# Performance work log

Measured on AMD Instinct MI355X. Metric: run time of the kernel, lower is better.

The kernel has to match this reference:

```python
import jax, jax.numpy as jnp
import numpy as np

B, S, E, D = 8, 2048, 1024, 128  # batch, seq (== max_span), embed_size, att_block_size


def setup_inputs() -> dict:
    key = jax.random.key(0)
    kx, kq, kk, kv = jax.random.split(key, 4)
    x = jax.random.normal(kx, (B, S, E), dtype=jnp.float32)
    # torch nn.Linear weight layout: [out_features, in_features]
    scale = 1.0 / np.sqrt(E)
    Wq = jax.random.normal(kq, (D, E), dtype=jnp.float32) * scale
    Wk = jax.random.normal(kk, (D, E), dtype=jnp.float32) * scale
    Wv = jax.random.normal(kv, (D, E), dtype=jnp.float32) * scale
    return {"x": x, "Wq": Wq, "Wk": Wk, "Wv": Wv}


def reference(x, Wq, Wk, Wv):
    # q/k/v projections: nn.Linear without bias -> x @ W.T
    q = jnp.einsum('bse,de->bsd', x, Wq)  # [B,S,D]
    k = jnp.einsum('bse,de->bsd', x, Wk)
    v = jnp.einsum('bse,de->bsd', x, Wv)

    scores = jnp.einsum('bqd,bkd->bqk', q, k)  # [B,S,S]
    # causal mask (tril): -inf above diagonal
    causal = jnp.tril(jnp.ones((S, S), dtype=bool))
    scores = jnp.where(causal, scores, -jnp.inf)
    # faithful to source: scores divided by sqrt(D) TWICE => effective 1/D
    scores = scores / jnp.float32(D)
    attn = jax.nn.softmax(scores, axis=-1)
    z = jnp.einsum('bqk,bkd->bqd', attn, v)  # [B,S,D]
    return z
```

## Files before the change

### kernel.cpp

```cpp
#include <hip/hip_runtime.h>
#include <cstdint>
#include <cstddef>

#define DEV __device__ __forceinline__

typedef float  f32x4  __attribute__((ext_vector_type(4)));
typedef __bf16 bf16x4 __attribute__((ext_vector_type(4)));
typedef __bf16 bf16x8 __attribute__((ext_vector_type(8)));

constexpr int B = 8, S = 2048, E = 1024, D = 128;
constexpr int M = B * S;

constexpr size_t WS_QKV    = (size_t)3 * M * D;
constexpr size_t WS_F32OFF = WS_QKV + (size_t)3 * D * E;
constexpr size_t WS_NEED   = WS_F32OFF * 2;
constexpr size_t WS_NEED2  = WS_F32OFF * 2 + ((size_t)M * D + M) * 4;
constexpr int    NZ4       = (M * D + M) / 4;

DEV int sniff_is_bf16(const uint32_t* w) {
  int lane = threadIdx.x & 63;
  uint32_t v = w[lane * 1001];
  int e = (v >> 7) & 0xff;
  unsigned long long b = __ballot(e >= 100 && e <= 140);
  return __popcll(b) >= 48;
}

DEV bf16x4 cvt4(float4 f) {
  bf16x4 r; r[0] = (__bf16)f.x; r[1] = (__bf16)f.y; r[2] = (__bf16)f.z; r[3] = (__bf16)f.w;
  return r;
}

DEV void glds16(const void* g, void* l) {
  __builtin_amdgcn_global_load_lds(
      (const __attribute__((address_space(1))) void*)g,
      (__attribute__((address_space(3))) void*)l, 16, 0, 0);
}

__global__ __launch_bounds__(256) void wcast_kernel(
    const void* __restrict__ xp, const void* __restrict__ wqp,
    const void* __restrict__ wkp, const void* __restrict__ wvp,
    unsigned short* __restrict__ wbf, float* __restrict__ zbuf, const int nz4) {
  const int is_b = sniff_is_bf16((const uint32_t*)xp);
  const int row = blockIdx.x;
  const void* src = row < 128 ? wqp : (row < 256 ? wkp : wvp);
  const int r = row & 127;
  const int t = threadIdx.x;
  if (is_b) {
    const uint2* s = (const uint2*)((const unsigned short*)src + (size_t)r * E) + t;
    *((uint2*)(wbf + (size_t)row * E) + t) = *s;
  } else {
    float4 f = *((const float4*)((const float*)src + (size_t)r * E) + t);
    *((bf16x4*)(wbf + (size_t)row * E) + t) = cvt4(f);
  }
  if (nz4) {
    float4 z = {0.f, 0.f, 0.f, 0.f};
    float4* zp = (float4*)zbuf;
    for (int i = blockIdx.x * 256 + t; i < nz4; i += 384 * 256) zp[i] = z;
  }
}

__global__ __launch_bounds__(512, 4) void proj_kernel(
    const void* __restrict__ xp, const void* __restrict__ wqp,
    const void* __restrict__ wkp, const void* __restrict__ wvp,
    const unsigned short* __restrict__ wbf, const int use_wbf,
    unsigned short* __restrict__ ws) {
  __shared__ __align__(16) unsigned short lds[(32 + 384) * 72];
  unsigned short* xbuf = lds;
  unsigned short* wbuf = lds + 32 * 72;

  const int is_b = sniff_is_bf16((const uint32_t*)xp);
  const int m0 = blockIdx.x * 32;

  const int t = threadIdx.x, lane = t & 63, w = t >> 6;
  const int n15 = lane & 15, quad = lane >> 4;
  const int rg = w >> 2, cg = w & 3;

  f32x4 acc[6] = {};
  const int sr = t >> 3, sc8 = (t & 7) * 8;
  const int wr = t >> 3;

  for (int it = 0; it < 16; ++it) {
    const int k0 = it * 64;
    __syncthreads();
    if (t < 256) {
      if (!is_b) {
        const float4* sx = (const float4*)((const float*)xp + (size_t)(m0 + sr) * E + k0 + sc8);
        *(bf16x4*)&xbuf[sr * 72 + sc8] = cvt4(sx[0]);
        *(bf16x4*)&xbuf[sr * 72 + sc8 + 4] = cvt4(sx[1]);
      } else {
        *(uint4*)&xbuf[sr * 72 + sc8] =
            *(const uint4*)((const unsigned short*)xp + (size_t)(m0 + sr) * E + k0 + sc8);
      }
    }
    if (use_wbf) {
#pragma unroll
      for (int j = 0; j < 6; ++j)
        *(uint4*)&wbuf[(j * 64 + wr) * 72 + sc8] =
            *(const uint4*)(wbf + (size_t)(j * 64 + wr) * E + k0 + sc8);
    } else if (!is_b) {
#pragma unroll
      for (int j = 0; j < 6; ++j) {
        const float* wsrc = (j < 2) ? (const float*)wqp : (j < 4) ? (const float*)wkp : (const float*)wvp;
        const int wrow = (j & 1) * 64 + wr;
        const float4* sw = (const float4*)(wsrc + (size_t)wrow * E + k0 + sc8);
        *(bf16x4*)&wbuf[(j * 64 + wr) * 72 + sc8] = cvt4(sw[0]);
        *(bf16x4*)&wbuf[(j * 64 + wr) * 72 + sc8 + 4] = cvt4(sw[1]);
      }
    } else {
#pragma unroll
      for (int j = 0; j < 6; ++j) {
        const unsigned short* wsrc = (j < 2) ? (const unsigned short*)wqp
                                   : (j < 4) ? (const unsigned short*)wkp
                                             : (const unsigned short*)wvp;
        const int wrow = (j & 1) * 64 + wr;
        *(uint4*)&wbuf[(j * 64 + wr) * 72 + sc8] =
            *(const uint4*)(wsrc + (size_t)wrow * E + k0 + sc8);
      }
    }
    __syncthreads();
#pragma unroll
    for (int ks = 0; ks < 2; ++ks) {
      bf16x8 a = *(const bf16x8*)&xbuf[(rg * 16 + n15) * 72 + ks * 32 + quad * 8];
#pragma unroll
      for (int nf = 0; nf < 6; ++nf) {
        bf16x8 bfr = *(const bf16x8*)&wbuf[(cg * 96 + nf * 16 + n15) * 72 + ks * 32 + quad * 8];
        acc[nf] = __builtin_amdgcn_mfma_f32_16x16x32_bf16(a, bfr, acc[nf], 0, 0, 0);
      }
    }
  }

  unsigned short* qws = ws;
  unsigned short* kws = ws + (size_t)M * D;
  unsigned short* vtw = ws + (size_t)2 * M * D;

  __syncthreads();
  unsigned short* tbuf = lds;
#pragma unroll
  for (int nf = 0; nf < 6; ++nf) {
    const int col = cg * 96 + nf * 16 + n15;
    const int self = col >> 7;
    if (self < 2) {
      unsigned short* dst = self ? kws : qws;
      const int gcol = col & 127;
#pragma unroll
      for (int rr = 0; rr < 4; ++rr) {
        const int grow = m0 + rg * 16 + quad * 4 + rr;
        ((__bf16*)dst)[(size_t)grow * D + gcol] = (__bf16)acc[nf][rr];
      }
    } else {
      const int vcol = col - 256;
#pragma unroll
      for (int rr = 0; rr < 4; ++rr)
        ((__bf16*)tbuf)[(rg * 16 + quad * 4 + rr) * 132 + vcol] = (__bf16)acc[nf][rr];
    }
  }
  __syncthreads();
  {
    const int dcol = t >> 2, mst = (t & 3) * 8;
    unsigned short tmp[8] __attribute__((aligned(16)));
#pragma unroll
    for (int j = 0; j < 8; ++j) tmp[j] = tbuf[(mst + j) * 132 + dcol];
    *(uint4*)&vtw[(size_t)dcol * M + m0 + mst] = *(const uint4*)&tmp[0];
  }
}

__global__ __launch_bounds__(256, 2) void attn_seg_kernel(
    const unsigned short* __restrict__ ws, float* __restrict__ ws2,
    float* __restrict__ lws) {
  __shared__ __align__(16) unsigned short kvbuf[2 * 16384];
  __shared__ __align__(16) unsigned short ldsP[4 * 640];

  const int bx = blockIdx.x;
  const int batch = bx & 7;
  const int seg = (bx >> 3) & 1;
  const int t16 = 63 - (bx >> 4);
  const int q0 = t16 * 32;

  const int nch = (q0 + 95) >> 6;
  const int c0 = seg ? ((nch + 1) >> 1) : 0;
  const int c1 = seg ? nch : ((nch + 1) >> 1);
  if (c0 >= c1) return;

  const int t = threadIdx.x, lane = t & 63, s = t >> 6;
  const int qg = s >> 1, kh = s & 1;
  const int n15 = lane & 15, quad = lane >> 4;

  const unsigned short* qws = ws;
  const unsigned short* kws = ws + (size_t)M * D;
  const unsigned short* vtw = ws + (size_t)2 * M * D;
  unsigned short* ldsPw = ldsP + s * 640;

  bf16x8 qf[4];
  {
    const size_t qbase = (size_t)(batch * S + q0 + qg * 16 + n15) * D;
#pragma unroll
    for (int ks = 0; ks < 4; ++ks)
      qf[ks] = *(const bf16x8*)&qws[qbase + ks * 32 + quad * 8];
  }

  const bf16x8 ones = {(__bf16)1.0f, (__bf16)1.0f, (__bf16)1.0f, (__bf16)1.0f,
                       (__bf16)1.0f, (__bf16)1.0f, (__bf16)1.0f, (__bf16)1.0f};

  f32x4 o[8] = {};
  f32x4 lacc = {};

  const int wrow = q0 + qg * 16 + 15;
  const int ncw = (wrow >= kh * 32) ? (((wrow - kh * 32) >> 6) + 1) : 0;

  const int r4 = lane >> 4, c16 = lane & 15;
  const int r8 = lane >> 3, c8 = lane & 7;
  const size_t kgbase = (size_t)(batch * S) * D;
  const size_t vgbase = (size_t)batch * S;

#define STAGE(j0c, b)                                                            \
  {                                                                              \
    unsigned short* kb_ = kvbuf + (b)*16384;                                     \
    unsigned short* vb_ = kb_ + 8192;                                            \
    _Pragma("unroll") for (int j = 0; j < 4; ++j) {                              \
      const int krow = s * 16 + j * 4 + r4;                                      \
      glds16(kws + kgbase + (size_t)((j0c) + krow) * D + ((c16 ^ (krow & 7)) << 3), \
             kb_ + (s * 16 + j * 4) * 128);                                      \
    }                                                                            \
    _Pragma("unroll") for (int j = 0; j < 4; ++j) {                              \
      const int dr = s * 32 + j * 8 + r8;                                        \
      glds16(vtw + (size_t)dr * M + vgbase + (j0c) + ((c8 ^ (dr & 7)) << 3),     \
             vb_ + (s * 32 + j * 8) * 64);                                       \
    }                                                                            \
  }

  STAGE(c0 * 64, c0 & 1);

  for (int c = c0; c < c1; ++c) {
    if (c + 1 < c1) {
      STAGE((c + 1) * 64, (c + 1) & 1);
      asm volatile("s_waitcnt vmcnt(8)" ::: "memory");
    } else {
      asm volatile("s_waitcnt vmcnt(0)" ::: "memory");
    }
    __builtin_amdgcn_s_barrier();

    if (c < ncw) {
      const unsigned short* kb = kvbuf + (c & 1) * 16384;
      const unsigned short* vb = kb + 8192;
      const int xsw = n15 & 7;

      f32x4 sc[2] = {};
      __builtin_amdgcn_s_setprio(1);
#pragma unroll
      for (int nt = 0; nt < 2; ++nt) {
        const int klrow = kh * 32 + nt * 16 + n15;
#pragma unroll
        for (int ks = 0; ks < 4; ++ks) {
          const bf16x8 ka = *(const bf16x8*)&kb[klrow * 128 + (((ks * 4 + quad) ^ xsw) << 3)];
          sc[nt] = __builtin_amdgcn_mfma_f32_16x16x32_bf16(ka, qf[ks], sc[nt], 0, 0, 0);
        }
      }
      __builtin_amdgcn_s_setprio(0);

      const int j0 = c * 64 + kh * 32;
      const bool maskc = (c == ncw - 1);
#pragma unroll
      for (int nt = 0; nt < 2; ++nt) {
        bf16x4 pv;
#pragma unroll
        for (int rr = 0; rr < 4; ++rr) {
          float v = sc[nt][rr] * (1.0f / 128.0f);
          if (maskc && (j0 + nt * 16 + quad * 4 + rr > q0 + qg * 16 + n15)) v = -1e30f;
          pv[rr] = (__bf16)__expf(v);
        }
        *(bf16x4*)&ldsPw[n15 * 40 + nt * 16 + quad * 4] = pv;
      }

      const bf16x8 pa = *(const bf16x8*)&ldsPw[n15 * 40 + quad * 8];
      __builtin_amdgcn_s_setprio(1);
#pragma unroll
      for (int dn = 0; dn < 8; ++dn) {
        const bf16x8 vfr =
            *(const bf16x8*)&vb[(dn * 16 + n15) * 64 + (((kh * 4 + quad) ^ xsw) << 3)];
        o[dn] = __builtin_amdgcn_mfma_f32_16x16x32_bf16(pa, vfr, o[dn], 0, 0, 0);
      }
      lacc = __builtin_amdgcn_mfma_f32_16x16x32_bf16(pa, ones, lacc, 0, 0, 0);
      __builtin_amdgcn_s_setprio(0);
    }

    __builtin_amdgcn_s_barrier();
  }
#undef STAGE

  float* obase = ws2 + (size_t)(batch * S + q0) * D;
#pragma unroll
  for (int dn = 0; dn < 8; ++dn)
#pragma unroll
    for (int rr = 0; rr < 4; ++rr)
      atomicAdd(&obase[(size_t)(qg * 16 + quad * 4 + rr) * D + dn * 16 + n15], o[dn][rr]);
  if (n15 == 0)
#pragma unroll
    for (int rr = 0; rr < 4; ++rr)
      atomicAdd(&lws[batch * S + q0 + qg * 16 + quad * 4 + rr], lacc[rr]);
}

__global__ __launch_bounds__(256, 2) void attn_kernel(
    const void* __restrict__ xp, const unsigned short* __restrict__ ws,
    void* __restrict__ outp) {
  __shared__ __align__(16) unsigned short kvbuf[2 * 16384];
  __shared__ __align__(16) unsigned short ldsP[4 * 640];
  __shared__ float lbuf[32];
  __shared__ int cnt2[2];

  const int is_b = sniff_is_bf16((const uint32_t*)xp);
  const int bx = blockIdx.x;
  const int batch = bx & 7;
  const int g8 = (bx & 255) >> 3;
  const int t16 = (bx < 256) ? (63 - g8) : g8;
  const int q0 = t16 * 32;
  const int t = threadIdx.x, lane = t & 63, s = t >> 6;
  const int qg = s >> 1, kh = s & 1;
  const int n15 = lane & 15, quad = lane >> 4;

  const unsigned short* qws = ws;
  const unsigned short* kws = ws + (size_t)M * D;
  const unsigned short* vtw = ws + (size_t)2 * M * D;
  unsigned short* ldsPw = ldsP + s * 640;

  if (t < 2) cnt2[t] = 0;

  bf16x8 qf[4];
  {
    const size_t qbase = (size_t)(batch * S + q0 + qg * 16 + n15) * D;
#pragma unroll
    for (int ks = 0; ks < 4; ++ks)
      qf[ks] = *(const bf16x8*)&qws[qbase + ks * 32 + quad * 8];
  }

  const bf16x8 ones = {(__bf16)1.0f, (__bf16)1.0f, (__bf16)1.0f, (__bf16)1.0f,
                       (__bf16)1.0f, (__bf16)1.0f, (__bf16)1.0f, (__bf16)1.0f};

  f32x4 o[8] = {};
  f32x4 lacc = {};

  const int nch = (q0 + 95) >> 6;
  const int wrow = q0 + qg * 16 + 15;
  const int ncw = (wrow >= kh * 32) ? (((wrow - kh * 32) >> 6) + 1) : 0;

  const int r4 = lane >> 4, c16 = lane & 15;
  const int r8 = lane >> 3, c8 = lane & 7;
  const size_t kgbase = (size_t)(batch * S) * D;
  const size_t vgbase = (size_t)batch * S;

#define STAGE(j0c, b)                                                            \
  {                                                                              \
    unsigned short* kb_ = kvbuf + (b)*16384;                                     \
    unsigned short* vb_ = kb_ + 8192;                                            \
    _Pragma("unroll") for (int j = 0; j < 4; ++j) {                              \
      const int krow = s * 16 + j * 4 + r4;                                      \
      glds16(kws + kgbase + (size_t)((j0c) + krow) * D + ((c16 ^ (krow & 7)) << 3), \
             kb_ + (s * 16 + j * 4) * 128);                                      \
    }                                                                            \
    _Pragma("unroll") for (int j = 0; j < 4; ++j) {                              \
      const int dr = s * 32 + j * 8 + r8;                                        \
      glds16(vtw + (size_t)dr * M + vgbase + (j0c) + ((c8 ^ (dr & 7)) << 3),     \
             vb_ + (s * 32 + j * 8) * 64);                                       \
    }                                                                            \
  }

  STAGE(0, 0);

  for (int c = 0; c < nch; ++c) {
    if (c + 1 < nch) {
      STAGE((c + 1) * 64, (c + 1) & 1);
      asm volatile("s_waitcnt vmcnt(8)" ::: "memory");
    } else {
      asm volatile("s_waitcnt vmcnt(0)" ::: "memory");
    }
    __builtin_amdgcn_s_barrier();

    if (c < ncw) {
      const unsigned short* kb = kvbuf + (c & 1) * 16384;
      const unsigned short* vb = kb + 8192;
      const int xsw = n15 & 7;

      f32x4 sc[2] = {};
      __builtin_amdgcn_s_setprio(1);
#pragma unroll
      for (int nt = 0; nt < 2; ++nt) {
        const int klrow = kh * 32 + nt * 16 + n15;
#pragma unroll
        for (int ks = 0; ks < 4; ++ks) {
          const bf16x8 ka = *(const bf16x8*)&kb[klrow * 128 + (((ks * 4 + quad) ^ xsw) << 3)];
          sc[nt] = __builtin_amdgcn_mfma_f32_16x16x32_bf16(ka, qf[ks], sc[nt], 0, 0, 0);
        }
      }
      __builtin_amdgcn_s_setprio(0);

      const int j0 = c * 64 + kh * 32;
      const bool maskc = (c == ncw - 1);
#pragma unroll
      for (int nt = 0; nt < 2; ++nt) {
        bf16x4 pv;
#pragma unroll
        for (int rr = 0; rr < 4; ++rr) {
          float v = sc[nt][rr] * (1.0f / 128.0f);
          if (maskc && (j0 + nt * 16 + quad * 4 + rr > q0 + qg * 16 + n15)) v = -1e30f;
          pv[rr] = (__bf16)__expf(v);
        }
        *(bf16x4*)&ldsPw[n15 * 40 + nt * 16 + quad * 4] = pv;
      }

      const bf16x8 pa = *(const bf16x8*)&ldsPw[n15 * 40 + quad * 8];
      __builtin_amdgcn_s_setprio(1);
#pragma unroll
      for (int dn = 0; dn < 8; ++dn) {
        const bf16x8 vfr =
            *(const bf16x8*)&vb[(dn * 16 + n15) * 64 + (((kh * 4 + quad) ^ xsw) << 3)];
        o[dn] = __builtin_amdgcn_mfma_f32_16x16x32_bf16(pa, vfr, o[dn], 0, 0, 0);
      }
      lacc = __builtin_amdgcn_mfma_f32_16x16x32_bf16(pa, ones, lacc, 0, 0, 0);
      __builtin_amdgcn_s_setprio(0);
    }

    __builtin_amdgcn_s_barrier();
  }
#undef STAGE

  __syncthreads();

  float* Obuf = (float*)kvbuf;
  if (kh == 0) {
#pragma unroll
    for (int dn = 0; dn < 8; ++dn)
#pragma unroll
      for (int rr = 0; rr < 4; ++rr)
        Obuf[(qg * 16 + quad * 4 + rr) * 132 + dn * 16 + n15] = o[dn][rr];
    if (n15 == 0)
#pragma unroll
      for (int rr = 0; rr < 4; ++rr)
        lbuf[qg * 16 + quad * 4 + rr] = lacc[rr];
    asm volatile("" ::: "memory");
    if (lane == 0) atomicAdd(&cnt2[qg], 1);
  } else {
    while (__hip_atomic_load(&cnt2[qg], __ATOMIC_RELAXED, __HIP_MEMORY_SCOPE_WORKGROUP) < 1)
      __builtin_amdgcn_s_sleep(1);
    asm volatile("" ::: "memory");
#pragma unroll
    for (int dn = 0; dn < 8; ++dn)
#pragma unroll
      for (int rr = 0; rr < 4; ++rr)
        atomicAdd(&Obuf[(qg * 16 + quad * 4 + rr) * 132 + dn * 16 + n15], o[dn][rr]);
    if (n15 == 0)
#pragma unroll
      for (int rr = 0; rr < 4; ++rr)
        atomicAdd(&lbuf[qg * 16 + quad * 4 + rr], lacc[rr]);
    if (lane == 0) atomicAdd(&cnt2[qg], 1);
  }
  while (__hip_atomic_load(&cnt2[0], __ATOMIC_RELAXED, __HIP_MEMORY_SCOPE_WORKGROUP) < 2 ||
         __hip_atomic_load(&cnt2[1], __ATOMIC_RELAXED, __HIP_MEMORY_SCOPE_WORKGROUP) < 2)
    __builtin_amdgcn_s_sleep(1);
  asm volatile("" ::: "memory");

  {
    const int row = t >> 3, cb = (t & 7) * 16;
    const float invl = 1.0f / lbuf[row];
    const size_t grow = (size_t)(batch * S + q0 + row) * D;
    if (is_b) {
#pragma unroll
      for (int i = 0; i < 16; ++i)
        ((__bf16*)outp)[grow + cb + i] = (__bf16)(Obuf[row * 132 + cb + i] * invl);
    } else {
#pragma unroll
      for (int i = 0; i < 16; ++i)
        ((float*)outp)[grow + cb + i] = Obuf[row * 132 + cb + i] * invl;
    }
  }
}

__global__ __launch_bounds__(256) void finalize_kernel(
    const void* __restrict__ xp, const float* __restrict__ ws2,
    const float* __restrict__ lws, void* __restrict__ outp) {
  const int is_b = sniff_is_bf16((const uint32_t*)xp);
  const size_t g = ((size_t)blockIdx.x * 256 + threadIdx.x) * 8;
  const int m = (int)(g >> 7);
  const float invl = 1.0f / lws[m];
  float4 a = *(const float4*)(ws2 + g);
  float4 b2 = *(const float4*)(ws2 + g + 4);
  if (is_b) {
    bf16x8 r;
    r[0] = (__bf16)(a.x * invl);  r[1] = (__bf16)(a.y * invl);
    r[2] = (__bf16)(a.z * invl);  r[3] = (__bf16)(a.w * invl);
    r[4] = (__bf16)(b2.x * invl); r[5] = (__bf16)(b2.y * invl);
    r[6] = (__bf16)(b2.z * invl); r[7] = (__bf16)(b2.w * invl);
    *(bf16x8*)((__bf16*)outp + g) = r;
  } else {
    float4 ra = {a.x * invl, a.y * invl, a.z * invl, a.w * invl};
    float4 rb = {b2.x * invl, b2.y * invl, b2.z * invl, b2.w * invl};
    *(float4*)((float*)outp + g) = ra;
    *(float4*)((float*)outp + g + 4) = rb;
  }
}

extern "C" void kernel_launch(void* const* d_in, const int* in_sizes, int n_in,
                              void* d_out, int out_size, void* d_ws, size_t ws_size,
                              hipStream_t stream) {
  (void)in_sizes; (void)n_in; (void)out_size;
  const void* x  = d_in[0];
  const void* wq = d_in[1];
  const void* wk = d_in[2];
  const void* wv = d_in[3];
  unsigned short* ws = (unsigned short*)d_ws;
  unsigned short* wbf = ws + WS_QKV;
  float* ws2 = (float*)(ws + WS_F32OFF);
  float* lws = ws2 + (size_t)M * D;
  const int use_wbf = (ws_size >= WS_NEED) ? 1 : 0;
  const int use_seg = (ws_size >= WS_NEED2) ? 1 : 0;

  if (use_wbf)
    wcast_kernel<<<dim3(384), dim3(256), 0, stream>>>(x, wq, wk, wv, wbf, ws2,
                                                      use_seg ? NZ4 : 0);
  proj_kernel<<<dim3(512), dim3(512), 0, stream>>>(x, wq, wk, wv, wbf, use_wbf, ws);
  if (use_seg) {
    attn_seg_kernel<<<dim3(1024), dim3(256), 0, stream>>>(ws, ws2, lws);
    finalize_kernel<<<dim3(1024), dim3(256), 0, stream>>>(x, ws2, lws, d_out);
  } else {
    attn_kernel<<<dim3(512), dim3(256), 0, stream>>>(x, ws, d_out);
  }
}
```

Before: 174.8 us.

## Double-buffer projection GEMM with direct global-to-LDS loads and XOR swizzle

Rewrites the QKV projection main loop for the bf16-input fast path. It now double-buffers the x and weight tiles in LDS using direct global-to-LDS loads (glds16), with vmcnt waits and raw barriers, so the next tile's loads overlap the current MFMAs. LDS padding is replaced by an XOR swizzle to avoid bank conflicts. The larger shared buffer lowers the occupancy hint from 4 to 2 blocks per CU, which may reduce latency hiding. The fast path only runs when the input is detected as bf16; fp32 inputs take the swizzled single-buffer fallback.

```diff
diff --git a/kernel.cpp b/kernel.cpp
--- a/kernel.cpp
+++ b/kernel.cpp
@@ -59,82 +59,121 @@
   }
 }
 
-__global__ __launch_bounds__(512, 4) void proj_kernel(
+__global__ __launch_bounds__(512, 2) void proj_kernel(
     const void* __restrict__ xp, const void* __restrict__ wqp,
     const void* __restrict__ wkp, const void* __restrict__ wvp,
     const unsigned short* __restrict__ wbf, const int use_wbf,
     unsigned short* __restrict__ ws) {
-  __shared__ __align__(16) unsigned short lds[(32 + 384) * 72];
-  unsigned short* xbuf = lds;
-  unsigned short* wbuf = lds + 32 * 72;
+  __shared__ __align__(16) unsigned short xw[2 * 26624];
 
   const int is_b = sniff_is_bf16((const uint32_t*)xp);
   const int m0 = blockIdx.x * 32;
 
-  const int t = threadIdx.x, lane = t & 63, w = t >> 6;
+  const int t = threadIdx.x, lane = t & 63, s = t >> 6;
   const int n15 = lane & 15, quad = lane >> 4;
-  const int rg = w >> 2, cg = w & 3;
+  const int rg = s >> 2, cg = s & 3;
+  const int xsw = n15 & 7;
 
   f32x4 acc[6] = {};
-  const int sr = t >> 3, sc8 = (t & 7) * 8;
-  const int wr = t >> 3;
-
-  for (int it = 0; it < 16; ++it) {
-    const int k0 = it * 64;
-    __syncthreads();
-    if (t < 256) {
-      if (!is_b) {
-        const float4* sx = (const float4*)((const float*)xp + (size_t)(m0 + sr) * E + k0 + sc8);
-        *(bf16x4*)&xbuf[sr * 72 + sc8] = cvt4(sx[0]);
-        *(bf16x4*)&xbuf[sr * 72 + sc8 + 4] = cvt4(sx[1]);
+
+#define PMFMA(xb_, wb_)                                                         \
+  {                                                                             \
+    _Pragma("unroll") for (int ks = 0; ks < 2; ++ks) {                          \
+      bf16x8 a = *(const bf16x8*)&(xb_)[(rg * 16 + n15) * 64 +                  \
+                                        (((ks * 4 + quad) ^ xsw) << 3)];        \
+      _Pragma("unroll") for (int nf = 0; nf < 6; ++nf) {                        \
+        const int wc = cg * 96 + nf * 16 + n15;                                 \
+        bf16x8 bb = *(const bf16x8*)&(wb_)[wc * 64 +                            \
+                                           (((ks * 4 + quad) ^ xsw) << 3)];     \
+        acc[nf] = __builtin_amdgcn_mfma_f32_16x16x32_bf16(a, bb, acc[nf], 0, 0, 0); \
+      }                                                                         \
+    }                                                                           \
+  }
+
+  if (is_b && use_wbf) {
+#define PSTAGE(k0_, b_)                                                          \
+  {                                                                              \
+    unsigned short* xd = xw + (b_) * 26624 + s * 256;                            \
+    unsigned short* wd = xw + (b_) * 26624 + 2048;                               \
+    if (lane < 32) {                                                             \
+      const int xr = s * 4 + (lane >> 3);                                        \
+      glds16((const unsigned short*)xp + (size_t)(m0 + xr) * E + (k0_) +         \
+                 (((lane & 7) ^ (xr & 7)) << 3),                                 \
+             xd);                                                                \
+    }                                                                            \
+    _Pragma("unroll") for (int j = 0; j < 6; ++j) {                              \
+      const int wr_ = (s * 6 + j) * 8 + (lane >> 3);                             \
+      glds16(wbf + (size_t)wr_ * E + (k0_) + (((lane & 7) ^ (wr_ & 7)) << 3),    \
+             wd + (s * 6 + j) * 512);                                            \
+    }                                                                            \
+  }
+    PSTAGE(0, 0);
+    for (int it = 0; it < 16; ++it) {
+      if (it + 1 < 16) {
+        PSTAGE((it + 1) * 64, (it + 1) & 1);
+        asm volatile("s_waitcnt vmcnt(7)" ::: "memory");
       } else {
-        *(uint4*)&xbuf[sr * 72 + sc8] =
-            *(const uint4*)((const unsigned short*)xp + (size_t)(m0 + sr) * E + k0 + sc8);
-      }
-    }
-    if (use_wbf) {
-#pragma unroll
-      for (int j = 0; j < 6; ++j)
-        *(uint4*)&wbuf[(j * 64 + wr) * 72 + sc8] =
-            *(const uint4*)(wbf + (size_t)(j * 64 + wr) * E + k0 + sc8);
-    } else if (!is_b) {
+        asm volatile("s_waitcnt vmcnt(0)" ::: "memory");
+      }
+      __builtin_amdgcn_s_barrier();
+      const unsigned short* xb_ = xw + (it & 1) * 26624;
+      const unsigned short* wb_ = xb_ + 2048;
+      __builtin_amdgcn_s_setprio(1);
+      PMFMA(xb_, wb_);
+      __builtin_amdgcn_s_setprio(0);
+      __builtin_amdgcn_s_barrier();
+    }
+#undef PSTAGE
+  } else {
+    unsigned short* xb_ = xw;
+    unsigned short* wb_ = xw + 2048;
+    const int fr = t >> 3, fs = t & 7;
+    for (int it = 0; it < 16; ++it) {
+      const int k0 = it * 64;
+      __syncthreads();
+      if (t < 256) {
+        const int pos = fr * 64 + ((fs ^ (fr & 7)) << 3);
+        if (!is_b) {
+          const float* sx = (const float*)xp + (size_t)(m0 + fr) * E + k0 + fs * 8;
+          *(bf16x4*)&xb_[pos] = cvt4(*(const float4*)sx);
+          *(bf16x4*)&xb_[pos + 4] = cvt4(*(const float4*)(sx + 4));
+        } else {
+          *(uint4*)&xb_[pos] =
+              *(const uint4*)((const unsigned short*)xp + (size_t)(m0 + fr) * E + k0 + fs * 8);
+        }
+      }
 #pragma unroll
       for (int j = 0; j < 6; ++j) {
-        const float* wsrc = (j < 2) ? (const float*)wqp : (j < 4) ? (const float*)wkp : (const float*)wvp;
-        const int wrow = (j & 1) * 64 + wr;
-        const float4* sw = (const float4*)(wsrc + (size_t)wrow * E + k0 + sc8);
-        *(bf16x4*)&wbuf[(j * 64 + wr) * 72 + sc8] = cvt4(sw[0]);
-        *(bf16x4*)&wbuf[(j * 64 + wr) * 72 + sc8 + 4] = cvt4(sw[1]);
-      }
-    } else {
-#pragma unroll
-      for (int j = 0; j < 6; ++j) {
-        const unsigned short* wsrc = (j < 2) ? (const unsigned short*)wqp
-                                   : (j < 4) ? (const unsigned short*)wkp
-                                             : (const unsigned short*)wvp;
-        const int wrow = (j & 1) * 64 + wr;
-        *(uint4*)&wbuf[(j * 64 + wr) * 72 + sc8] =
-            *(const uint4*)(wsrc + (size_t)wrow * E + k0 + sc8);
-      }
-    }
-    __syncthreads();
-#pragma unroll
-    for (int ks = 0; ks < 2; ++ks) {
-      bf16x8 a = *(const bf16x8*)&xbuf[(rg * 16 + n15) * 72 + ks * 32 + quad * 8];
-#pragma unroll
-      for (int nf = 0; nf < 6; ++nf) {
-        bf16x8 bfr = *(const bf16x8*)&wbuf[(cg * 96 + nf * 16 + n15) * 72 + ks * 32 + quad * 8];
-        acc[nf] = __builtin_amdgcn_mfma_f32_16x16x32_bf16(a, bfr, acc[nf], 0, 0, 0);
-      }
-    }
-  }
+        const int wr_ = j * 64 + fr;
+        const int pos = wr_ * 64 + ((fs ^ (wr_ & 7)) << 3);
+        if (use_wbf) {
+          *(uint4*)&wb_[pos] = *(const uint4*)(wbf + (size_t)wr_ * E + k0 + fs * 8);
+        } else if (!is_b) {
+          const float* wsrc = (j < 2) ? (const float*)wqp : (j < 4) ? (const float*)wkp : (const float*)wvp;
+          const int wrow = (j & 1) * 64 + fr;
+          const float* sw = wsrc + (size_t)wrow * E + k0 + fs * 8;
+          *(bf16x4*)&wb_[pos] = cvt4(*(const float4*)sw);
+          *(bf16x4*)&wb_[pos + 4] = cvt4(*(const float4*)(sw + 4));
+        } else {
+          const unsigned short* wsrc = (j < 2) ? (const unsigned short*)wqp
+                                     : (j < 4) ? (const unsigned short*)wkp
+                                               : (const unsigned short*)wvp;
+          const int wrow = (j & 1) * 64 + fr;
+          *(uint4*)&wb_[pos] = *(const uint4*)(wsrc + (size_t)wrow * E + k0 + fs * 8);
+        }
+      }
+      __syncthreads();
+      PMFMA(xb_, wb_);
+    }
+  }
+#undef PMFMA
 
   unsigned short* qws = ws;
   unsigned short* kws = ws + (size_t)M * D;
   unsigned short* vtw = ws + (size_t)2 * M * D;
 
   __syncthreads();
-  unsigned short* tbuf = lds;
+  unsigned short* tbuf = xw;
 #pragma unroll
   for (int nf = 0; nf < 6; ++nf) {
     const int col = cg * 96 + nf * 16 + n15;
```

After: 226.6 us. +29.6%, slower.

## Retile QKV projection to 64x192 blocks and rebalance attention segments

Applied to the files above, without the earlier changes.

The projection kernel now gives each block 64 rows by 192 output columns with a 128-wide K step and XOR-swizzled LDS, replacing 32-row blocks that each covered all 384 columns. The attention segment kernel moves to 512-thread blocks covering 64 query rows, with a schedule that splits each query tile into segments of up to eight KV chunks. It skips atomics for waves that have no work. The aim is better load balance across causal tiles and less redundant K/V staging, at the cost of more blocks writing atomically into the same outputs and a lower occupancy bound on the projection kernel.

```diff
diff --git a/kernel.cpp b/kernel.cpp
--- a/kernel.cpp
+++ b/kernel.cpp
@@ -59,72 +59,78 @@
   }
 }
 
-__global__ __launch_bounds__(512, 4) void proj_kernel(
+__global__ __launch_bounds__(512, 2) void proj_kernel(
     const void* __restrict__ xp, const void* __restrict__ wqp,
     const void* __restrict__ wkp, const void* __restrict__ wvp,
     const unsigned short* __restrict__ wbf, const int use_wbf,
     unsigned short* __restrict__ ws) {
-  __shared__ __align__(16) unsigned short lds[(32 + 384) * 72];
+  __shared__ __align__(16) unsigned short lds[(64 + 192) * 128];
   unsigned short* xbuf = lds;
-  unsigned short* wbuf = lds + 32 * 72;
+  unsigned short* wbuf = lds + 64 * 128;
 
   const int is_b = sniff_is_bf16((const uint32_t*)xp);
-  const int m0 = blockIdx.x * 32;
-
-  const int t = threadIdx.x, lane = t & 63, w = t >> 6;
+  const int bx = blockIdx.x;
+  const int m0 = (bx >> 1) * 64;
+  const int n0 = (bx & 1) * 192;
+
+  const int t = threadIdx.x, lane = t & 63, s = t >> 6;
   const int n15 = lane & 15, quad = lane >> 4;
-  const int rg = w >> 2, cg = w & 3;
+  const int rg = s >> 1, cg = s & 1;
+  const int xsw = n15 & 7;
 
   f32x4 acc[6] = {};
-  const int sr = t >> 3, sc8 = (t & 7) * 8;
-  const int wr = t >> 3;
-
-  for (int it = 0; it < 16; ++it) {
-    const int k0 = it * 64;
+  const int sr = t >> 3, sl = t & 7;
+
+  for (int it = 0; it < 8; ++it) {
+    const int k0 = it * 128;
     __syncthreads();
-    if (t < 256) {
-      if (!is_b) {
-        const float4* sx = (const float4*)((const float*)xp + (size_t)(m0 + sr) * E + k0 + sc8);
-        *(bf16x4*)&xbuf[sr * 72 + sc8] = cvt4(sx[0]);
-        *(bf16x4*)&xbuf[sr * 72 + sc8 + 4] = cvt4(sx[1]);
+    if (!is_b) {
+      const float* sx = (const float*)xp + (size_t)(m0 + sr) * E + k0;
+#pragma unroll
+      for (int g = 0; g < 2; ++g) {
+        const int slot = sl + g * 8;
+        const int pos = sr * 128 + ((slot ^ (sr & 7)) << 3);
+        *(bf16x4*)&xbuf[pos] = cvt4(*(const float4*)(sx + slot * 8));
+        *(bf16x4*)&xbuf[pos + 4] = cvt4(*(const float4*)(sx + slot * 8 + 4));
+      }
+    } else {
+      const unsigned short* sx = (const unsigned short*)xp + (size_t)(m0 + sr) * E + k0;
+#pragma unroll
+      for (int g = 0; g < 2; ++g) {
+        const int slot = sl + g * 8;
+        *(uint4*)&xbuf[sr * 128 + ((slot ^ (sr & 7)) << 3)] = *(const uint4*)(sx + slot * 8);
+      }
+    }
+#pragma unroll
+    for (int jj = 0; jj < 6; ++jj) {
+      const int wr = (jj >> 1) * 64 + sr;
+      const int gr = n0 + wr;
+      const int slot = sl + (jj & 1) * 8;
+      const int pos = wr * 128 + ((slot ^ (wr & 7)) << 3);
+      if (use_wbf) {
+        *(uint4*)&wbuf[pos] = *(const uint4*)(wbf + (size_t)gr * E + k0 + slot * 8);
+      } else if (!is_b) {
+        const float* wsrc = (gr < 128) ? (const float*)wqp
+                          : (gr < 256) ? (const float*)wkp : (const float*)wvp;
+        const float* sw = wsrc + (size_t)(gr & 127) * E + k0 + slot * 8;
+        *(bf16x4*)&wbuf[pos] = cvt4(*(const float4*)sw);
+        *(bf16x4*)&wbuf[pos + 4] = cvt4(*(const float4*)(sw + 4));
       } else {
-        *(uint4*)&xbuf[sr * 72 + sc8] =
-            *(const uint4*)((const unsigned short*)xp + (size_t)(m0 + sr) * E + k0 + sc8);
-      }
-    }
-    if (use_wbf) {
-#pragma unroll
-      for (int j = 0; j < 6; ++j)
-        *(uint4*)&wbuf[(j * 64 + wr) * 72 + sc8] =
-            *(const uint4*)(wbf + (size_t)(j * 64 + wr) * E + k0 + sc8);
-    } else if (!is_b) {
-#pragma unroll
-      for (int j = 0; j < 6; ++j) {
-        const float* wsrc = (j < 2) ? (const float*)wqp : (j < 4) ? (const float*)wkp : (const float*)wvp;
-        const int wrow = (j & 1) * 64 + wr;
-        const float4* sw = (const float4*)(wsrc + (size_t)wrow * E + k0 + sc8);
-        *(bf16x4*)&wbuf[(j * 64 + wr) * 72 + sc8] = cvt4(sw[0]);
-        *(bf16x4*)&wbuf[(j * 64 + wr) * 72 + sc8 + 4] = cvt4(sw[1]);
-      }
-    } else {
-#pragma unroll
-      for (int j = 0; j < 6; ++j) {
-        const unsigned short* wsrc = (j < 2) ? (const unsigned short*)wqp
-                                   : (j < 4) ? (const unsigned short*)wkp
-                                             : (const unsigned short*)wvp;
-        const int wrow = (j & 1) * 64 + wr;
-        *(uint4*)&wbuf[(j * 64 + wr) * 72 + sc8] =
-            *(const uint4*)(wsrc + (size_t)wrow * E + k0 + sc8);
+        const unsigned short* wsrc = (gr < 128) ? (const unsigned short*)wqp
+                                   : (gr < 256) ? (const unsigned short*)wkp
+                                                : (const unsigned short*)wvp;
+        *(uint4*)&wbuf[pos] = *(const uint4*)(wsrc + (size_t)(gr & 127) * E + k0 + slot * 8);
       }
     }
     __syncthreads();
 #pragma unroll
-    for (int ks = 0; ks < 2; ++ks) {
-      bf16x8 a = *(const bf16x8*)&xbuf[(rg * 16 + n15) * 72 + ks * 32 + quad * 8];
+    for (int ks = 0; ks < 4; ++ks) {
+      bf16x8 a = *(const bf16x8*)&xbuf[(rg * 16 + n15) * 128 + (((ks * 4 + quad) ^ xsw) << 3)];
 #pragma unroll
       for (int nf = 0; nf < 6; ++nf) {
-        bf16x8 bfr = *(const bf16x8*)&wbuf[(cg * 96 + nf * 16 + n15) * 72 + ks * 32 + quad * 8];
-        acc[nf] = __builtin_amdgcn_mfma_f32_16x16x32_bf16(a, bfr, acc[nf], 0, 0, 0);
+        bf16x8 bb = *(const bf16x8*)&wbuf[(cg * 96 + nf * 16 + n15) * 128 +
+                                          (((ks * 4 + quad) ^ xsw) << 3)];
+        acc[nf] = __builtin_amdgcn_mfma_f32_16x16x32_bf16(a, bb, acc[nf], 0, 0, 0);
       }
     }
   }
@@ -137,7 +143,7 @@
   unsigned short* tbuf = lds;
 #pragma unroll
   for (int nf = 0; nf < 6; ++nf) {
-    const int col = cg * 96 + nf * 16 + n15;
+    const int col = n0 + cg * 96 + nf * 16 + n15;
     const int self = col >> 7;
     if (self < 2) {
       unsigned short* dst = self ? kws : qws;
@@ -154,32 +160,35 @@
         ((__bf16*)tbuf)[(rg * 16 + quad * 4 + rr) * 132 + vcol] = (__bf16)acc[nf][rr];
     }
   }
-  __syncthreads();
-  {
-    const int dcol = t >> 2, mst = (t & 3) * 8;
-    unsigned short tmp[8] __attribute__((aligned(16)));
-#pragma unroll
-    for (int j = 0; j < 8; ++j) tmp[j] = tbuf[(mst + j) * 132 + dcol];
+  if (n0) {
+    __syncthreads();
+    const int dcol = t >> 2, mst = (t & 3) * 16;
+    unsigned short tmp[16] __attribute__((aligned(16)));
+#pragma unroll
+    for (int j = 0; j < 16; ++j) tmp[j] = tbuf[(mst + j) * 132 + dcol];
     *(uint4*)&vtw[(size_t)dcol * M + m0 + mst] = *(const uint4*)&tmp[0];
-  }
-}
-
-__global__ __launch_bounds__(256, 2) void attn_seg_kernel(
+    *(uint4*)&vtw[(size_t)dcol * M + m0 + mst + 8] = *(const uint4*)&tmp[8];
+  }
+}
+
+__global__ __launch_bounds__(512, 2) void attn_seg_kernel(
     const unsigned short* __restrict__ ws, float* __restrict__ ws2,
     float* __restrict__ lws) {
   __shared__ __align__(16) unsigned short kvbuf[2 * 16384];
-  __shared__ __align__(16) unsigned short ldsP[4 * 640];
+  __shared__ __align__(16) unsigned short ldsP[8 * 640];
 
   const int bx = blockIdx.x;
   const int batch = bx & 7;
-  const int seg = (bx >> 3) & 1;
-  const int t16 = 63 - (bx >> 4);
-  const int q0 = t16 * 32;
-
-  const int nch = (q0 + 95) >> 6;
-  const int c0 = seg ? ((nch + 1) >> 1) : 0;
-  const int c1 = seg ? nch : ((nch + 1) >> 1);
-  if (c0 >= c1) return;
+  const int m = bx >> 3;
+  int T, k;
+  if (m < 32)      { T = 31 - (m >> 2); k = m & 3; }
+  else if (m < 56) { int mm = m - 32; T = 23 - mm / 3; k = mm % 3; }
+  else if (m < 72) { int mm = m - 56; T = 15 - (mm >> 1); k = mm & 1; }
+  else             { T = 7 - (m - 72); k = 0; }
+  const int q0 = T * 64;
+  const int nch = T + 1;
+  const int c0 = k * 8;
+  const int c1 = (c0 + 8 < nch) ? (c0 + 8) : nch;
 
   const int t = threadIdx.x, lane = t & 63, s = t >> 6;
   const int qg = s >> 1, kh = s & 1;
@@ -216,15 +225,15 @@
   {                                                                              \
     unsigned short* kb_ = kvbuf + (b)*16384;                                     \
     unsigned short* vb_ = kb_ + 8192;                                            \
-    _Pragma("unroll") for (int j = 0; j < 4; ++j) {                              \
-      const int krow = s * 16 + j * 4 + r4;                                      \
+    _Pragma("unroll") for (int j = 0; j < 2; ++j) {                              \
+      const int krow = s * 8 + j * 4 + r4;                            \
       glds16(kws + kgbase + (size_t)((j0c) + krow) * D + ((c16 ^ (krow & 7)) << 3), \
-             kb_ + (s * 16 + j * 4) * 128);                                      \
+             kb_ + (s * 8 + j * 4) * 128);                                       \
     }                                                                            \
-    _Pragma("unroll") for (int j = 0; j < 4; ++j) {                              \
-      const int dr = s * 32 + j * 8 + r8;                                        \
+    _Pragma("unroll") for (int j = 0; j < 2; ++j) {                              \
+      const int dr = s * 16 + j * 8 + r8;                            \
       glds16(vtw + (size_t)dr * M + vgbase + (j0c) + ((c8 ^ (dr & 7)) << 3),     \
-             vb_ + (s * 32 + j * 8) * 64);                                       \
+             vb_ + (s * 16 + j * 8) * 64);                                       \
     }                                                                            \
   }
 
@@ -233,7 +242,7 @@
   for (int c = c0; c < c1; ++c) {
     if (c + 1 < c1) {
       STAGE((c + 1) * 64, (c + 1) & 1);
-      asm volatile("s_waitcnt vmcnt(8)" ::: "memory");
+      asm volatile("s_waitcnt vmcnt(4)" ::: "memory");
     } else {
       asm volatile("s_waitcnt vmcnt(0)" ::: "memory");
     }
@@ -287,16 +296,18 @@
   }
 #undef STAGE
 
-  float* obase = ws2 + (size_t)(batch * S + q0) * D;
-#pragma unroll
-  for (int dn = 0; dn < 8; ++dn)
-#pragma unroll
-    for (int rr = 0; rr < 4; ++rr)
-      atomicAdd(&obase[(size_t)(qg * 16 + quad * 4 + rr) * D + dn * 16 + n15], o[dn][rr]);
-  if (n15 == 0)
-#pragma unroll
-    for (int rr = 0; rr < 4; ++rr)
-      atomicAdd(&lws[batch * S + q0 + qg * 16 + quad * 4 + rr], lacc[rr]);
+  if (ncw > c0) {
+    float* obase = ws2 + (size_t)(batch * S + q0) * D;
+#pragma unroll
+    for (int dn = 0; dn < 8; ++dn)
+#pragma unroll
+      for (int rr = 0; rr < 4; ++rr)
+        atomicAdd(&obase[(size_t)(qg * 16 + quad * 4 + rr) * D + dn * 16 + n15], o[dn][rr]);
+    if (n15 == 0)
+#pragma unroll
+      for (int rr = 0; rr < 4; ++rr)
+        atomicAdd(&lws[batch * S + q0 + qg * 16 + quad * 4 + rr], lacc[rr]);
+  }
 }
 
 __global__ __launch_bounds__(256, 2) void attn_kernel(
@@ -517,7 +528,7 @@
                                                       use_seg ? NZ4 : 0);
   proj_kernel<<<dim3(512), dim3(512), 0, stream>>>(x, wq, wk, wv, wbf, use_wbf, ws);
   if (use_seg) {
-    attn_seg_kernel<<<dim3(1024), dim3(256), 0, stream>>>(ws, ws2, lws);
+    attn_seg_kernel<<<dim3(640), dim3(512), 0, stream>>>(ws, ws2, lws);
     finalize_kernel<<<dim3(1024), dim3(256), 0, stream>>>(x, ws2, lws, d_out);
   } else {
     attn_kernel<<<dim3(512), dim3(256), 0, stream>>>(x, ws, d_out);
```

New measurement: 198.5 us. 13.6% more time.

## Replace global atomic split-K accumulation with per-segment buffers and in-block LDS reduction

Applied to the files above, without the earlier changes.

Each attention segment block now reduces its two key-half waves in shared memory and writes its partial O and row-sum to a dedicated per-segment buffer with plain vector stores. Global float atomics and the zero-fill of the accumulation buffer in the weight-cast kernel go away. The finalize kernel sums the two segment partials when a second segment exists. This removes many scattered global atomics and a large memset, in exchange for twice the workspace, an extra read in finalize, and an intra-block spin-wait handshake.

```diff
diff --git a/kernel.cpp b/kernel.cpp
--- a/kernel.cpp
+++ b/kernel.cpp
@@ -14,8 +14,7 @@
 constexpr size_t WS_QKV    = (size_t)3 * M * D;
 constexpr size_t WS_F32OFF = WS_QKV + (size_t)3 * D * E;
 constexpr size_t WS_NEED   = WS_F32OFF * 2;
-constexpr size_t WS_NEED2  = WS_F32OFF * 2 + ((size_t)M * D + M) * 4;
-constexpr int    NZ4       = (M * D + M) / 4;
+constexpr size_t WS_NEED2  = WS_F32OFF * 2 + ((size_t)2 * M * D + 2 * M) * 4;
 
 DEV int sniff_is_bf16(const uint32_t* w) {
   int lane = threadIdx.x & 63;
@@ -39,7 +38,7 @@
 __global__ __launch_bounds__(256) void wcast_kernel(
     const void* __restrict__ xp, const void* __restrict__ wqp,
     const void* __restrict__ wkp, const void* __restrict__ wvp,
-    unsigned short* __restrict__ wbf, float* __restrict__ zbuf, const int nz4) {
+    unsigned short* __restrict__ wbf) {
   const int is_b = sniff_is_bf16((const uint32_t*)xp);
   const int row = blockIdx.x;
   const void* src = row < 128 ? wqp : (row < 256 ? wkp : wvp);
@@ -52,11 +51,6 @@
     float4 f = *((const float4*)((const float*)src + (size_t)r * E) + t);
     *((bf16x4*)(wbf + (size_t)row * E) + t) = cvt4(f);
   }
-  if (nz4) {
-    float4 z = {0.f, 0.f, 0.f, 0.f};
-    float4* zp = (float4*)zbuf;
-    for (int i = blockIdx.x * 256 + t; i < nz4; i += 384 * 256) zp[i] = z;
-  }
 }
 
 __global__ __launch_bounds__(512, 4) void proj_kernel(
@@ -165,10 +159,12 @@
 }
 
 __global__ __launch_bounds__(256, 2) void attn_seg_kernel(
-    const unsigned short* __restrict__ ws, float* __restrict__ ws2,
-    float* __restrict__ lws) {
+    const unsigned short* __restrict__ ws, float* __restrict__ o_a,
+    float* __restrict__ o_b, float* __restrict__ l_a, float* __restrict__ l_b) {
   __shared__ __align__(16) unsigned short kvbuf[2 * 16384];
   __shared__ __align__(16) unsigned short ldsP[4 * 640];
+  __shared__ float lbuf[32];
+  __shared__ int cnt2[2];
 
   const int bx = blockIdx.x;
   const int batch = bx & 7;
@@ -189,6 +185,8 @@
   const unsigned short* kws = ws + (size_t)M * D;
   const unsigned short* vtw = ws + (size_t)2 * M * D;
   unsigned short* ldsPw = ldsP + s * 640;
+
+  if (t < 2) cnt2[t] = 0;
 
   bf16x8 qf[4];
   {
@@ -287,16 +285,51 @@
   }
 #undef STAGE
 
-  float* obase = ws2 + (size_t)(batch * S + q0) * D;
-#pragma unroll
-  for (int dn = 0; dn < 8; ++dn)
-#pragma unroll
-    for (int rr = 0; rr < 4; ++rr)
-      atomicAdd(&obase[(size_t)(qg * 16 + quad * 4 + rr) * D + dn * 16 + n15], o[dn][rr]);
-  if (n15 == 0)
-#pragma unroll
-    for (int rr = 0; rr < 4; ++rr)
-      atomicAdd(&lws[batch * S + q0 + qg * 16 + quad * 4 + rr], lacc[rr]);
+  __syncthreads();
+
+  float* Obuf = (float*)kvbuf;
+  if (kh == 0) {
+#pragma unroll
+    for (int dn = 0; dn < 8; ++dn)
+#pragma unroll
+      for (int rr = 0; rr < 4; ++rr)
+        Obuf[(qg * 16 + quad * 4 + rr) * 132 + dn * 16 + n15] = o[dn][rr];
+    if (n15 == 0)
+#pragma unroll
+      for (int rr = 0; rr < 4; ++rr)
+        lbuf[qg * 16 + quad * 4 + rr] = lacc[rr];
+    asm volatile("" ::: "memory");
+    if (lane == 0) atomicAdd(&cnt2[qg], 1);
+  } else {
+    while (__hip_atomic_load(&cnt2[qg], __ATOMIC_RELAXED, __HIP_MEMORY_SCOPE_WORKGROUP) < 1)
+      __builtin_amdgcn_s_sleep(1);
+    asm volatile("" ::: "memory");
+#pragma unroll
+    for (int dn = 0; dn < 8; ++dn)
+#pragma unroll
+      for (int rr = 0; rr < 4; ++rr)
+        atomicAdd(&Obuf[(qg * 16 + quad * 4 + rr) * 132 + dn * 16 + n15], o[dn][rr]);
+    if (n15 == 0)
+#pragma unroll
+      for (int rr = 0; rr < 4; ++rr)
+        atomicAdd(&lbuf[qg * 16 + quad * 4 + rr], lacc[rr]);
+    if (lane == 0) atomicAdd(&cnt2[qg], 1);
+  }
+  while (__hip_atomic_load(&cnt2[0], __ATOMIC_RELAXED, __HIP_MEMORY_SCOPE_WORKGROUP) < 2 ||
+         __hip_atomic_load(&cnt2[1], __ATOMIC_RELAXED, __HIP_MEMORY_SCOPE_WORKGROUP) < 2)
+    __builtin_amdgcn_s_sleep(1);
+  asm volatile("" ::: "memory");
+
+  {
+    float* od = seg ? o_b : o_a;
+    float* ld = seg ? l_b : l_a;
+    const int row = t >> 3, cb = (t & 7) * 16;
+    const size_t grow = (size_t)(batch * S + q0 + row) * D;
+#pragma unroll
+    for (int i = 0; i < 16; i += 4)
+      *(float4*)&od[grow + cb + i] = *(const float4*)&Obuf[row * 132 + cb + i];
+    if (t < 32) ld[batch * S + q0 + t] = lbuf[t];
+  }
 }
 
 __global__ __launch_bounds__(256, 2) void attn_kernel(
@@ -474,24 +507,37 @@
 }
 
 __global__ __launch_bounds__(256) void finalize_kernel(
-    const void* __restrict__ xp, const float* __restrict__ ws2,
-    const float* __restrict__ lws, void* __restrict__ outp) {
+    const void* __restrict__ xp, const float* __restrict__ o_a,
+    const float* __restrict__ o_b, const float* __restrict__ l_a,
+    const float* __restrict__ l_b, void* __restrict__ outp) {
   const int is_b = sniff_is_bf16((const uint32_t*)xp);
   const size_t g = ((size_t)blockIdx.x * 256 + threadIdx.x) * 8;
   const int m = (int)(g >> 7);
-  const float invl = 1.0f / lws[m];
-  float4 a = *(const float4*)(ws2 + g);
-  float4 b2 = *(const float4*)(ws2 + g + 4);
+  const int q = m & (S - 1);
+  const int t16 = q >> 5;
+  const int nch = (t16 * 32 + 95) >> 6;
+  const int has2 = (((nch + 1) >> 1) < nch) ? 1 : 0;
+
+  float l = l_a[m] + (has2 ? l_b[m] : 0.0f);
+  const float invl = 1.0f / l;
+  float4 a0 = *(const float4*)(o_a + g);
+  float4 a1 = *(const float4*)(o_a + g + 4);
+  if (has2) {
+    float4 b0 = *(const float4*)(o_b + g);
+    float4 b1 = *(const float4*)(o_b + g + 4);
+    a0.x += b0.x; a0.y += b0.y; a0.z += b0.z; a0.w += b0.w;
+    a1.x += b1.x; a1.y += b1.y; a1.z += b1.z; a1.w += b1.w;
+  }
   if (is_b) {
     bf16x8 r;
-    r[0] = (__bf16)(a.x * invl);  r[1] = (__bf16)(a.y * invl);
-    r[2] = (__bf16)(a.z * invl);  r[3] = (__bf16)(a.w * invl);
-    r[4] = (__bf16)(b2.x * invl); r[5] = (__bf16)(b2.y * invl);
-    r[6] = (__bf16)(b2.z * invl); r[7] = (__bf16)(b2.w * invl);
+    r[0] = (__bf16)(a0.x * invl); r[1] = (__bf16)(a0.y * invl);
+    r[2] = (__bf16)(a0.z * invl); r[3] = (__bf16)(a0.w * invl);
+    r[4] = (__bf16)(a1.x * invl); r[5] = (__bf16)(a1.y * invl);
+    r[6] = (__bf16)(a1.z * invl); r[7] = (__bf16)(a1.w * invl);
     *(bf16x8*)((__bf16*)outp + g) = r;
   } else {
-    float4 ra = {a.x * invl, a.y * invl, a.z * invl, a.w * invl};
-    float4 rb = {b2.x * invl, b2.y * invl, b2.z * invl, b2.w * invl};
+    float4 ra = {a0.x * invl, a0.y * invl, a0.z * invl, a0.w * invl};
+    float4 rb = {a1.x * invl, a1.y * invl, a1.z * invl, a1.w * invl};
     *(float4*)((float*)outp + g) = ra;
     *(float4*)((float*)outp + g + 4) = rb;
   }
@@ -507,18 +553,19 @@
   const void* wv = d_in[3];
   unsigned short* ws = (unsigned short*)d_ws;
   unsigned short* wbf = ws + WS_QKV;
-  float* ws2 = (float*)(ws + WS_F32OFF);
-  float* lws = ws2 + (size_t)M * D;
+  float* o_a = (float*)(ws + WS_F32OFF);
+  float* o_b = o_a + (size_t)M * D;
+  float* l_a = o_b + (size_t)M * D;
+  float* l_b = l_a + M;
   const int use_wbf = (ws_size >= WS_NEED) ? 1 : 0;
   const int use_seg = (ws_size >= WS_NEED2) ? 1 : 0;
 
   if (use_wbf)
-    wcast_kernel<<<dim3(384), dim3(256), 0, stream>>>(x, wq, wk, wv, wbf, ws2,
-                                                      use_seg ? NZ4 : 0);
+    wcast_kernel<<<dim3(384), dim3(256), 0, stream>>>(x, wq, wk, wv, wbf);
   proj_kernel<<<dim3(512), dim3(512), 0, stream>>>(x, wq, wk, wv, wbf, use_wbf, ws);
   if (use_seg) {
-    attn_seg_kernel<<<dim3(1024), dim3(256), 0, stream>>>(ws, ws2, lws);
-    finalize_kernel<<<dim3(1024), dim3(256), 0, stream>>>(x, ws2, lws, d_out);
+    attn_seg_kernel<<<dim3(1024), dim3(256), 0, stream>>>(ws, o_a, o_b, l_a, l_b);
+    finalize_kernel<<<dim3(1024), dim3(256), 0, stream>>>(x, o_a, o_b, l_a, l_b, d_out);
   } else {
     attn_kernel<<<dim3(512), dim3(256), 0, stream>>>(x, ws, d_out);
   }
```

Result: slower. 178.9 us (+2.4%).
